# Kernel tuning notes

Measured on AMD Instinct MI355X. Metric: run time of the kernel, lower is better.

The kernel has to match this reference:

```python
import jax, jax.numpy as jnp
from jax import lax
import numpy as np

K = 256   # kernel_size == hidden channels (Haar basis size)
S = 16    # stride
BN_EPS = 1e-5


def _haar_matrix_unnorm(n):
    if n == 2:
        return np.array([[1.0, 1.0], [1.0, -1.0]])
    prev = _haar_matrix_unnorm(n // 2)
    top = np.kron(prev, np.array([1.0, 1.0]))
    bot = np.kron(np.eye(n // 2), np.array([1.0, -1.0]))
    return np.concatenate((top, bot))


def haar_matrix(n):
    h = _haar_matrix_unnorm(n)
    return h / np.linalg.norm(h, axis=1, keepdims=True)


def setup_inputs() -> dict:
    key = jax.random.key(0)
    ks = jax.random.split(key, 8)
    B, T = 64, 32768
    haar = jnp.asarray(haar_matrix(K), dtype=jnp.float32)          # [K, K]
    x = jax.random.normal(ks[0], (B, 1, T), dtype=jnp.float32)
    return {
        "x": x,
        # BitwiseConv1d(1, K, K, stride=S, padding=K)
        "conv_w": haar[:, None, :],                                 # [K, 1, K] (OIH)
        "conv_b": 0.01 * jax.random.normal(ks[1], (K,), dtype=jnp.float32),
        "conv_gate": jax.random.uniform(ks[2], (K, 1, K), dtype=jnp.float32),
        "conv_scale": jnp.ones((K,), dtype=jnp.float32),            # adaptive per-out-channel scale
        # BatchNorm1d(K)
        "bn_gamma": jnp.ones((K,), dtype=jnp.float32),
        "bn_beta": jnp.zeros((K,), dtype=jnp.float32),
        # BitwiseConvTranspose1d(K, 1, K, stride=S)
        "ct_w": haar.T[:, None, :],                                 # [K(in), 1(out), K] (IOH, torch layout)
        "ct_b": 0.01 * jax.random.normal(ks[3], (1,), dtype=jnp.float32),
        "ct_gate": jax.random.uniform(ks[4], (K, 1, K), dtype=jnp.float32),
        "ct_scale": jnp.ones((1,), dtype=jnp.float32),
    }


def _forward(x, conv_w, conv_b, conv_gate, conv_scale, bn_gamma, bn_beta,
             ct_w, ct_b, ct_gate, ct_scale):
    T = x.shape[2]
    # --- BitwiseConv1d: gated weights (in_bin/weight_bin = identity) ---
    # gate binarization maps gate -> (gate + 1) / 2, multiplied into weights
    w = conv_w * (conv_gate + 1.0) * 0.5                            # [K,1,K]
    h = lax.conv_general_dilated(
        x, w, window_strides=(S,), padding=[(K, K)],
        dimension_numbers=("NCH", "OIH", "NCH"))                  # [B,K,L]
    h = conv_scale[None, :, None] * (h + conv_b[None, :, None])    # adaptive scaling
    # --- ReLU then BatchNorm1d (training-mode batch statistics) ---
    h = jax.nn.relu(h)
    mu = jnp.mean(h, axis=(0, 2), keepdims=True)
    var = jnp.mean((h - mu) ** 2, axis=(0, 2), keepdims=True)
    h = (h - mu) * lax.rsqrt(var + BN_EPS)
    h = h * bn_gamma[None, :, None] + bn_beta[None, :, None]
    # --- BitwiseConvTranspose1d: gated weights, expressed as dilated conv ---
    wt = ct_w * (ct_gate + 1.0) * 0.5                               # [K_in, 1, K]
    # torch IOH -> regular-conv OIH with kernel flipped
    wr = jnp.flip(jnp.transpose(wt, (1, 0, 2)), axis=-1)            # [1, K, K]
    y = lax.conv_general_dilated(
        h, wr, window_strides=(1,), padding=[(K - 1, K - 1)],
        lhs_dilation=(S,), dimension_numbers=("NCH", "OIH", "NCH"))
    y = ct_scale[None, :, None] * (y + ct_b[None, :, None])
    # crop: out[:, :, K : T + K]
    return y[:, :, K:T + K]


def reference(x, conv_w, conv_b, conv_gate, conv_scale, bn_gamma, bn_beta,
              ct_w, ct_b, ct_gate, ct_scale):
    return _forward(x, conv_w, conv_b, conv_gate, conv_scale, bn_gamma, bn_beta,
                    ct_w, ct_b, ct_gate, ct_scale)
```

## Files before the change

kernel.cpp:

```cpp
#include <hip/hip_runtime.h>
#include <hip/hip_bf16.h>

#define BB 64
#define TT 32768
#define KK 256
#define LL 2065
#define NLT 9
#define NPART (BB*NLT)
#define NJ 19
#define HBSTR 72
#define NPT3 8

typedef __attribute__((ext_vector_type(8))) short short8;
typedef __attribute__((ext_vector_type(4))) float f32x4;
typedef __attribute__((ext_vector_type(4))) int int4v;
typedef __attribute__((ext_vector_type(2))) unsigned int uint2v;

__device__ __forceinline__ unsigned short f2bf(float f) {
    unsigned u = __builtin_bit_cast(unsigned, f);
    unsigned r = (u + 0x7FFFu + ((u >> 16) & 1u)) >> 16;
    return (unsigned short)r;
}
__device__ __forceinline__ unsigned pkbf(float a, float b) {
    unsigned r;
    asm("v_cvt_pk_bf16_f32 %0, %1, %2" : "=v"(r) : "v"(a), "v"(b));
    return r;
}
__device__ __forceinline__ void gload_lds16(const void* g, void* l) {
    __builtin_amdgcn_global_load_lds(
        (const __attribute__((address_space(1))) unsigned int*)g,
        (__attribute__((address_space(3))) unsigned int*)l, 16, 0, 0);
}

__global__ void k0_w1f(const float* __restrict__ cw, const float* __restrict__ cgt,
                       unsigned short* __restrict__ W1f)
{
    int idx = blockIdx.x*256 + threadIdx.x;
    int lane = idx & 63, ntL = (idx>>6)&7, kk = (idx>>9)&7, half = idx>>12;
    int o = half*128 + ntL*16 + (lane&15);
    int kbase = kk*32 + ((lane>>4)<<3);
    short8 v;
    #pragma unroll
    for (int i = 0; i < 8; ++i) {
        int gi = o*KK + kbase + i;
        v[i] = (short)f2bf(cw[gi]*(cgt[gi]+1.0f)*0.5f);
    }
    *(short8*)(W1f + (size_t)idx*8) = v;
}

__global__ __launch_bounds__(256, 3)
void k1_conv(const float* __restrict__ x, const float* __restrict__ cs,
             const float* __restrict__ cb, const unsigned short* __restrict__ W1f,
             unsigned short* __restrict__ hout,
             float* __restrict__ psum, float* __restrict__ psq)
{
    __shared__ __align__(16) char smem[13056 + 32768];
    char* xwinb = smem;
    char* wbuf  = smem + 13056;
    unsigned short* hb = (unsigned short*)smem;
    float* redS = (float*)(smem + 36864);
    float* redQ = (float*)(smem + 36864 + 1024);

    const int tid   = threadIdx.x;
    const int q     = blockIdx.x & 3;
    const int ltile = blockIdx.x >> 2;
    const int b     = blockIdx.y;
    const int l0    = ltile * 256;
    const long pos0 = (long)l0*16 - 256;
    const int lane  = tid & 63;
    const int w     = tid >> 6;

    {
        #pragma unroll
        for (int it = 0; it < 8; ++it) {
            int ci = w*8 + it;
            int kk = ci >> 2, ntl = ci & 3;
            size_t so = (size_t)((((q>>1)*8 + kk)*8 + (q&1)*4 + ntl))*1024;
            gload_lds16((const char*)W1f + so + lane*16, wbuf + ci*1024);
        }
    }
    {
        const float* xs = x + (size_t)b*TT;
        for (int g = tid; g < 272; g += 256) {
            long base = pos0 + (long)g*16;
            unsigned uu[8];
            if (base >= 0 && base + 16 <= (long)TT) {
                const float4* xv = (const float4*)(xs + base);
                float4 a0 = xv[0], a1 = xv[1], a2 = xv[2], a3 = xv[3];
                uu[0] = pkbf(a0.x, a0.y); uu[1] = pkbf(a0.z, a0.w);
                uu[2] = pkbf(a1.x, a1.y); uu[3] = pkbf(a1.z, a1.w);
                uu[4] = pkbf(a2.x, a2.y); uu[5] = pkbf(a2.z, a2.w);
                uu[6] = pkbf(a3.x, a3.y); uu[7] = pkbf(a3.z, a3.w);
            } else {
                #pragma unroll
                for (int m = 0; m < 16; m += 2) {
                    long p = base + m;
                    float f0 = (p   >= 0 && p   < TT) ? xs[p]   : 0.0f;
                    float f1 = (p+1 >= 0 && p+1 < TT) ? xs[p+1] : 0.0f;
                    uu[m>>1] = pkbf(f0, f1);
                }
            }
            int4v w0 = { (int)uu[0], (int)uu[1], (int)uu[2], (int)uu[3] };
            int4v w1 = { (int)uu[4], (int)uu[5], (int)uu[6], (int)uu[7] };
            *(int4v*)(xwinb + 48*g)      = w0;
            *(int4v*)(xwinb + 48*g + 16) = w1;
        }
    }
    __syncthreads();

    f32x4 acc[4][4];
    #pragma unroll
    for (int mt = 0; mt < 4; ++mt)
        #pragma unroll
        for (int nt = 0; nt < 4; ++nt) acc[mt][nt] = (f32x4){0.f,0.f,0.f,0.f};

    const int gq = lane >> 4;
    const int Gt = 16*gq + 16*(gq>>1);
    const int abase = 48*((w<<6) + (lane & 15)) + Gt;

    #pragma unroll
    for (int kk = 0; kk < 8; ++kk) {
        short8 bfx[4], afw[4];
        #pragma unroll
        for (int nt = 0; nt < 4; ++nt)
            bfx[nt] = *(const short8*)(xwinb + abase + nt*768 + kk*96);
        #pragma unroll
        for (int mt = 0; mt < 4; ++mt)
            afw[mt] = *(const short8*)(wbuf + (kk*4 + mt)*1024 + lane*16);
        __builtin_amdgcn_s_setprio(1);
        #pragma unroll
        for (int mt = 0; mt < 4; ++mt)
            #pragma unroll
            for (int nt = 0; nt < 4; ++nt)
                acc[mt][nt] = __builtin_amdgcn_mfma_f32_16x16x32_bf16(afw[mt], bfx[nt], acc[mt][nt], 0, 0, 0);
        __builtin_amdgcn_s_setprio(0);
    }
    __syncthreads();

    const int c0 = q*64;
    const int g  = lane >> 4;
    const int li = lane & 15;
    #pragma unroll
    for (int mt = 0; mt < 4; ++mt) {
        int cq = c0 + mt*16 + g*4;
        f32x4 cs4 = *(const f32x4*)&cs[cq];
        f32x4 cb4 = *(const f32x4*)&cb[cq];
        f32x4 s4 = (f32x4){0.f,0.f,0.f,0.f};
        f32x4 q4 = (f32x4){0.f,0.f,0.f,0.f};
        #pragma unroll
        for (int nt = 0; nt < 4; ++nt) {
            int lloc = (w<<6) + nt*16 + li;
            f32x4 hv;
            #pragma unroll
            for (int rr = 0; rr < 4; ++rr)
                hv[rr] = fmaxf(cs4[rr]*(acc[mt][nt][rr] + cb4[rr]), 0.0f);
            uint2v pkv = { pkbf(hv[0], hv[1]), pkbf(hv[2], hv[3]) };
            *(uint2v*)(hb + lloc*HBSTR + mt*16 + g*4) = pkv;
            if (l0 + lloc < LL) { s4 += hv; q4 += hv*hv; }
        }
        #pragma unroll
        for (int d = 1; d < 16; d <<= 1) {
            #pragma unroll
            for (int rr = 0; rr < 4; ++rr) {
                s4[rr] += __shfl_xor(s4[rr], d);
                q4[rr] += __shfl_xor(q4[rr], d);
            }
        }
        if (li == 0) {
            *(f32x4*)&redS[((w*4 + mt)*4 + g)*4] = s4;
            *(f32x4*)&redQ[((w*4 + mt)*4 + g)*4] = q4;
        }
    }
    __syncthreads();

    {
        const int rsub = tid >> 3;
        const int cpos = tid & 7;
        #pragma unroll
        for (int it = 0; it < 8; ++it) {
            int row = it*32 + rsub;
            int l = l0 + row;
            if (l < LL) {
                int4v v = *(const int4v*)(hb + row*HBSTR + cpos*8);
                *(int4v*)(hout + (((size_t)(b*LL + l)) << 8) + q*64 + cpos*8) = v;
            }
        }
    }
    if (tid < 64) {
        int mt = tid >> 4, gg = (tid >> 2) & 3, rr = tid & 3;
        float s = 0.f, qq = 0.f;
        #pragma unroll
        for (int wv = 0; wv < 4; ++wv) {
            s  += redS[((wv*4 + mt)*4 + gg)*4 + rr];
            qq += redQ[((wv*4 + mt)*4 + gg)*4 + rr];
        }
        int c = c0 + tid;
        int slot = b*NLT + ltile;
        psum[c*NPART + slot] = s;
        psq [c*NPART + slot] = qq;
    }
}

__global__ __launch_bounds__(256)
void k2_bn(const float* __restrict__ psum, const float* __restrict__ psq,
           const float* __restrict__ bng, const float* __restrict__ bnb,
           const float* __restrict__ ctw, const float* __restrict__ ctg,
           const float* __restrict__ ctscale,
           float* __restrict__ W3s, float* __restrict__ SWS)
{
    __shared__ double rs[4], rq[4];
    __shared__ float s_a, s_bc;
    __shared__ float swl[256];
    const int c = blockIdx.x;
    const int tid = threadIdx.x;
    double s = 0.0, q = 0.0;
    for (int i = tid; i < NPART; i += 256) {
        s += (double)psum[c*NPART + i];
        q += (double)psq [c*NPART + i];
    }
    for (int off = 32; off > 0; off >>= 1) {
        s += __shfl_down(s, off);
        q += __shfl_down(q, off);
    }
    if ((tid & 63) == 0) { rs[tid >> 6] = s; rq[tid >> 6] = q; }
    __syncthreads();
    if (tid == 0) {
        double st = rs[0]+rs[1]+rs[2]+rs[3];
        double qt = rq[0]+rq[1]+rq[2]+rq[3];
        const double cnt = (double)BB * (double)LL;
        double mu = st / cnt;
        double var = qt / cnt - mu*mu;
        float rsig = (float)(1.0 / sqrt(var + 1e-5));
        float a = bng[c] * rsig;
        s_a = a;
        s_bc = bnb[c] - (float)mu * a;
    }
    __syncthreads();
    float a = s_a, bc = s_bc, scl = ctscale[0];
    int gi = c*KK + tid;
    float wt = ctw[gi] * (ctg[gi] + 1.0f) * 0.5f;
    W3s[tid*KK + c] = scl * a * wt;
    swl[tid] = wt * bc;
    __syncthreads();
    if (tid < 16) {
        float acc2 = 0.0f;
        #pragma unroll
        for (int d = 0; d < 16; ++d) acc2 += swl[d*16 + tid];
        SWS[c*16 + tid] = acc2;
    }
}

__global__ void k2b_const(const float* __restrict__ SWS, const float* __restrict__ ctb,
                          const float* __restrict__ ctscale, float* __restrict__ C2)
{
    int r = threadIdx.x;
    if (r < 16) {
        float s = 0.0f;
        for (int c = 0; c < 256; ++c) s += SWS[c*16 + r];
        C2[r] = ctscale[0] * (s + ctb[0]);
    }
}

__global__ void k2c_b2f(const float* __restrict__ W3s, unsigned short* __restrict__ B2f)
{
    int idx = blockIdx.x*256 + threadIdx.x;
    int lane = idx & 63;
    int ntG  = (idx>>6) & 3;
    int kk   = (idx>>8) & 7;
    int j    = idx>>11;
    int c    = kk*32 + ((lane>>4)<<3);
    int r    = lane & 15;
    int d    = ntG + 15 - j;
    short8 v;
    if (d >= 0 && d <= 15) {
        const float* wr = W3s + (size_t)(16*d + r)*KK + c;
        #pragma unroll
        for (int i = 0; i < 8; ++i) v[i] = (short)f2bf(wr[i]);
    } else {
        #pragma unroll
        for (int i = 0; i < 8; ++i) v[i] = 0;
    }
    *(short8*)(B2f + (size_t)idx*8) = v;
}

__global__ __launch_bounds__(512, 1)
void k3_synth(const unsigned short* __restrict__ h, const unsigned short* __restrict__ B2f,
              const float* __restrict__ C2, float* __restrict__ out)
{
    __shared__ __align__(16) char As[272*512];
    const int tid  = threadIdx.x;
    const int lane = tid & 63;
    const int w    = tid >> 6;
    const int b    = blockIdx.y;
    const int P0   = blockIdx.x * 64;

    const char* hbase = (const char*)h + (((size_t)(b*LL) + 4*P0 + 1) << 9);

    {
        const int rl = lane >> 5;
        #pragma unroll
        for (int i = 0; i < 17; ++i) {
            int r0  = w*34 + i*2;
            int row = r0 + rl;
            int chunk = (lane & 31) ^ ((row >> 2) & 7);
            gload_lds16(hbase + (size_t)row*512 + chunk*16, As + r0*512);
        }
    }
    __syncthreads();

    const int ntG = w & 3;
    const int jh  = w >> 2;
    const int li  = lane & 15;
    const int gq  = lane >> 4;

    f32x4 acc[4];
    #pragma unroll
    for (int mt = 0; mt < 4; ++mt) acc[mt] = (f32x4){0.f,0.f,0.f,0.f};

    #pragma unroll 1
    for (int ji = 0; ji < 8; ++ji) {
        const int j = ntG + jh*8 + ji;
        short8 bfr[8];
        #pragma unroll
        for (int kk = 0; kk < 8; ++kk)
            bfr[kk] = *(const short8*)(B2f + (((size_t)(j*8 + kk)*4 + ntG)*64 + lane)*8);
        #pragma unroll
        for (int kk = 0; kk < 8; ++kk) {
            short8 af[4];
            #pragma unroll
            for (int mt = 0; mt < 4; ++mt) {
                int row = 64*mt + 4*li + j;
                int p = (kk*4 + gq) ^ ((row >> 2) & 7);
                af[mt] = *(const short8*)(As + row*512 + p*16);
            }
            __builtin_amdgcn_s_setprio(1);
            #pragma unroll
            for (int mt = 0; mt < 4; ++mt)
                acc[mt] = __builtin_amdgcn_mfma_f32_16x16x32_bf16(af[mt], bfr[kk], acc[mt], 0, 0, 0);
            __builtin_amdgcn_s_setprio(0);
        }
    }
    __syncthreads();

    float* red = (float*)As;
    #pragma unroll
    for (int mt = 0; mt < 4; ++mt) {
        int u = ntG*16 + li;
        #pragma unroll
        for (int rr = 0; rr < 4; ++rr) {
            int Pl = 16*mt + gq*4 + rr;
            red[jh*4352 + Pl*68 + u] = acc[mt][rr];
        }
    }
    __syncthreads();

    {
        const float c2v = C2[tid & 15];
        const int u  = tid & 63;
        const int Pb = tid >> 6;
        float* ob = out + (size_t)b*TT + (size_t)P0*64;
        #pragma unroll
        for (int it = 0; it < 8; ++it) {
            int P = it*8 + Pb;
            ob[P*64 + u] = red[P*68 + u] + red[4352 + P*68 + u] + c2v;
        }
    }
}

extern "C" void kernel_launch(void* const* d_in, const int* in_sizes, int n_in,
                              void* d_out, int out_size, void* d_ws, size_t ws_size,
                              hipStream_t stream)
{
    const float* x       = (const float*)d_in[0];
    const float* cw      = (const float*)d_in[1];
    const float* cb      = (const float*)d_in[2];
    const float* cgt     = (const float*)d_in[3];
    const float* cs      = (const float*)d_in[4];
    const float* bng     = (const float*)d_in[5];
    const float* bnb     = (const float*)d_in[6];
    const float* ctw     = (const float*)d_in[7];
    const float* ctb     = (const float*)d_in[8];
    const float* ctg     = (const float*)d_in[9];
    const float* ctscale = (const float*)d_in[10];
    float* out = (float*)d_out;

    char* ws = (char*)d_ws;
    size_t off = 0;
    unsigned short* h    = (unsigned short*)(ws + off); off += (size_t)BB*LL*KK*2;
    float* psum          = (float*)(ws + off);          off += (size_t)KK*NPART*4;
    float* psq           = (float*)(ws + off);          off += (size_t)KK*NPART*4;
    unsigned short* W1f  = (unsigned short*)(ws + off); off += 65536*2;
    float* W3s           = (float*)(ws + off);          off += (size_t)KK*KK*4;
    float* SWS           = (float*)(ws + off);          off += (size_t)KK*16*4;
    float* C2            = (float*)(ws + off);          off += 64;
    unsigned short* B2f  = (unsigned short*)(ws + off); off += (size_t)NJ*8*4*64*8*2;

    k0_w1f  <<<32, 256, 0, stream>>>(cw, cgt, W1f);
    k1_conv <<<dim3(36, BB), 256, 0, stream>>>(x, cs, cb, W1f, h, psum, psq);
    k2_bn   <<<KK, 256, 0, stream>>>(psum, psq, bng, bnb, ctw, ctg, ctscale, W3s, SWS);
    k2b_const<<<1, 64, 0, stream>>>(SWS, ctb, ctscale, C2);
    k2c_b2f <<<152, 256, 0, stream>>>(W3s, B2f);
    k3_synth<<<dim3(NPT3, BB), 512, 0, stream>>>(h, B2f, C2, out);
}
```

Before: 85.37 us.

## Widen conv tile to 128 channels per block and double-buffer synth weight loads

The first conv kernel now uses 512-thread blocks covering 128 output channels, so each x window is staged and converted once per two channel quarters instead of four. This halves the grid and the redundant x loads, at the cost of more LDS per block and lower occupancy. The synthesis kernel now double-buffers its per-j B fragments in registers, prefetching the next j while computing the current one, which raises register pressure.

After: 93.83 us. 1.1x slower.

```diff
diff --git a/kernel.cpp b/kernel.cpp
--- a/kernel.cpp
+++ b/kernel.cpp
@@ -8,7 +8,7 @@
 #define NLT 9
 #define NPART (BB*NLT)
 #define NJ 19
-#define HBSTR 72
+#define HBSTR 132
 #define NPT3 8
 
 typedef __attribute__((ext_vector_type(8))) short short8;
@@ -48,63 +48,63 @@
     *(short8*)(W1f + (size_t)idx*8) = v;
 }
 
-__global__ __launch_bounds__(256, 3)
+__global__ __launch_bounds__(512, 2)
 void k1_conv(const float* __restrict__ x, const float* __restrict__ cs,
              const float* __restrict__ cb, const unsigned short* __restrict__ W1f,
              unsigned short* __restrict__ hout,
              float* __restrict__ psum, float* __restrict__ psq)
 {
-    __shared__ __align__(16) char smem[13056 + 32768];
+    __shared__ __align__(16) char smem[13056 + 65536];
     char* xwinb = smem;
     char* wbuf  = smem + 13056;
     unsigned short* hb = (unsigned short*)smem;
-    float* redS = (float*)(smem + 36864);
-    float* redQ = (float*)(smem + 36864 + 1024);
+    float* redS = (float*)(smem + 67584);
+    float* redQ = (float*)(smem + 67584 + 2048);
 
     const int tid   = threadIdx.x;
-    const int q     = blockIdx.x & 3;
-    const int ltile = blockIdx.x >> 2;
+    const int half  = blockIdx.x & 1;
+    const int ltile = blockIdx.x >> 1;
     const int b     = blockIdx.y;
     const int l0    = ltile * 256;
     const long pos0 = (long)l0*16 - 256;
     const int lane  = tid & 63;
     const int w     = tid >> 6;
+    const int wq    = w >> 1;
+    const int wc    = w & 1;
 
     {
+        const char* wsrc = (const char*)(W1f + (size_t)half*32768);
         #pragma unroll
         for (int it = 0; it < 8; ++it) {
             int ci = w*8 + it;
-            int kk = ci >> 2, ntl = ci & 3;
-            size_t so = (size_t)((((q>>1)*8 + kk)*8 + (q&1)*4 + ntl))*1024;
-            gload_lds16((const char*)W1f + so + lane*16, wbuf + ci*1024);
-        }
-    }
-    {
+            gload_lds16(wsrc + ci*1024 + lane*16, wbuf + ci*1024);
+        }
+    }
+    if (tid < 272) {
         const float* xs = x + (size_t)b*TT;
-        for (int g = tid; g < 272; g += 256) {
-            long base = pos0 + (long)g*16;
-            unsigned uu[8];
-            if (base >= 0 && base + 16 <= (long)TT) {
-                const float4* xv = (const float4*)(xs + base);
-                float4 a0 = xv[0], a1 = xv[1], a2 = xv[2], a3 = xv[3];
-                uu[0] = pkbf(a0.x, a0.y); uu[1] = pkbf(a0.z, a0.w);
-                uu[2] = pkbf(a1.x, a1.y); uu[3] = pkbf(a1.z, a1.w);
-                uu[4] = pkbf(a2.x, a2.y); uu[5] = pkbf(a2.z, a2.w);
-                uu[6] = pkbf(a3.x, a3.y); uu[7] = pkbf(a3.z, a3.w);
-            } else {
-                #pragma unroll
-                for (int m = 0; m < 16; m += 2) {
-                    long p = base + m;
-                    float f0 = (p   >= 0 && p   < TT) ? xs[p]   : 0.0f;
-                    float f1 = (p+1 >= 0 && p+1 < TT) ? xs[p+1] : 0.0f;
-                    uu[m>>1] = pkbf(f0, f1);
-                }
+        const int g = tid;
+        long base = pos0 + (long)g*16;
+        unsigned uu[8];
+        if (base >= 0 && base + 16 <= (long)TT) {
+            const float4* xv = (const float4*)(xs + base);
+            float4 a0 = xv[0], a1 = xv[1], a2 = xv[2], a3 = xv[3];
+            uu[0] = pkbf(a0.x, a0.y); uu[1] = pkbf(a0.z, a0.w);
+            uu[2] = pkbf(a1.x, a1.y); uu[3] = pkbf(a1.z, a1.w);
+            uu[4] = pkbf(a2.x, a2.y); uu[5] = pkbf(a2.z, a2.w);
+            uu[6] = pkbf(a3.x, a3.y); uu[7] = pkbf(a3.z, a3.w);
+        } else {
+            #pragma unroll
+            for (int m = 0; m < 16; m += 2) {
+                long p = base + m;
+                float f0 = (p   >= 0 && p   < TT) ? xs[p]   : 0.0f;
+                float f1 = (p+1 >= 0 && p+1 < TT) ? xs[p+1] : 0.0f;
+                uu[m>>1] = pkbf(f0, f1);
             }
-            int4v w0 = { (int)uu[0], (int)uu[1], (int)uu[2], (int)uu[3] };
-            int4v w1 = { (int)uu[4], (int)uu[5], (int)uu[6], (int)uu[7] };
-            *(int4v*)(xwinb + 48*g)      = w0;
-            *(int4v*)(xwinb + 48*g + 16) = w1;
-        }
+        }
+        int4v w0 = { (int)uu[0], (int)uu[1], (int)uu[2], (int)uu[3] };
+        int4v w1 = { (int)uu[4], (int)uu[5], (int)uu[6], (int)uu[7] };
+        *(int4v*)(xwinb + 48*g)      = w0;
+        *(int4v*)(xwinb + 48*g + 16) = w1;
     }
     __syncthreads();
 
@@ -116,7 +116,7 @@
 
     const int gq = lane >> 4;
     const int Gt = 16*gq + 16*(gq>>1);
-    const int abase = 48*((w<<6) + (lane & 15)) + Gt;
+    const int abase = 48*((wq<<6) + (lane & 15)) + Gt;
 
     #pragma unroll
     for (int kk = 0; kk < 8; ++kk) {
@@ -126,7 +126,7 @@
             bfx[nt] = *(const short8*)(xwinb + abase + nt*768 + kk*96);
         #pragma unroll
         for (int mt = 0; mt < 4; ++mt)
-            afw[mt] = *(const short8*)(wbuf + (kk*4 + mt)*1024 + lane*16);
+            afw[mt] = *(const short8*)(wbuf + (kk*8 + wc*4 + mt)*1024 + lane*16);
         __builtin_amdgcn_s_setprio(1);
         #pragma unroll
         for (int mt = 0; mt < 4; ++mt)
@@ -137,26 +137,27 @@
     }
     __syncthreads();
 
-    const int c0 = q*64;
     const int g  = lane >> 4;
     const int li = lane & 15;
+    const bool interior = (l0 + 255 < LL);
     #pragma unroll
     for (int mt = 0; mt < 4; ++mt) {
-        int cq = c0 + mt*16 + g*4;
+        int cq = half*128 + wc*64 + mt*16 + g*4;
         f32x4 cs4 = *(const f32x4*)&cs[cq];
         f32x4 cb4 = *(const f32x4*)&cb[cq];
         f32x4 s4 = (f32x4){0.f,0.f,0.f,0.f};
         f32x4 q4 = (f32x4){0.f,0.f,0.f,0.f};
         #pragma unroll
         for (int nt = 0; nt < 4; ++nt) {
-            int lloc = (w<<6) + nt*16 + li;
+            int lloc = (wq<<6) + nt*16 + li;
             f32x4 hv;
             #pragma unroll
             for (int rr = 0; rr < 4; ++rr)
                 hv[rr] = fmaxf(cs4[rr]*(acc[mt][nt][rr] + cb4[rr]), 0.0f);
             uint2v pkv = { pkbf(hv[0], hv[1]), pkbf(hv[2], hv[3]) };
-            *(uint2v*)(hb + lloc*HBSTR + mt*16 + g*4) = pkv;
-            if (l0 + lloc < LL) { s4 += hv; q4 += hv*hv; }
+            *(uint2v*)(hb + lloc*HBSTR + wc*64 + mt*16 + g*4) = pkv;
+            if (interior) { s4 += hv; q4 += hv*hv; }
+            else if (l0 + lloc < LL) { s4 += hv; q4 += hv*hv; }
         }
         #pragma unroll
         for (int d = 1; d < 16; d <<= 1) {
@@ -174,27 +175,28 @@
     __syncthreads();
 
     {
-        const int rsub = tid >> 3;
-        const int cpos = tid & 7;
+        const int rsub = tid >> 4;
+        const int cpos = tid & 15;
         #pragma unroll
         for (int it = 0; it < 8; ++it) {
             int row = it*32 + rsub;
             int l = l0 + row;
             if (l < LL) {
                 int4v v = *(const int4v*)(hb + row*HBSTR + cpos*8);
-                *(int4v*)(hout + (((size_t)(b*LL + l)) << 8) + q*64 + cpos*8) = v;
+                *(int4v*)(hout + (((size_t)(b*LL + l)) << 8) + half*128 + cpos*8) = v;
             }
         }
     }
-    if (tid < 64) {
-        int mt = tid >> 4, gg = (tid >> 2) & 3, rr = tid & 3;
+    if (tid < 128) {
+        int wcc = tid >> 6, mt = (tid >> 4) & 3, gg = (tid >> 2) & 3, rr = tid & 3;
         float s = 0.f, qq = 0.f;
         #pragma unroll
-        for (int wv = 0; wv < 4; ++wv) {
-            s  += redS[((wv*4 + mt)*4 + gg)*4 + rr];
-            qq += redQ[((wv*4 + mt)*4 + gg)*4 + rr];
-        }
-        int c = c0 + tid;
+        for (int wqq = 0; wqq < 4; ++wqq) {
+            int wi = wqq*2 + wcc;
+            s  += redS[((wi*4 + mt)*4 + gg)*4 + rr];
+            qq += redQ[((wi*4 + mt)*4 + gg)*4 + rr];
+        }
+        int c = half*128 + tid;
         int slot = b*NLT + ltile;
         psum[c*NPART + slot] = s;
         psq [c*NPART + slot] = qq;
@@ -312,34 +314,53 @@
     const int jh  = w >> 2;
     const int li  = lane & 15;
     const int gq  = lane >> 4;
+    const int jbase = ntG + jh*8;
 
     f32x4 acc[4];
     #pragma unroll
     for (int mt = 0; mt < 4; ++mt) acc[mt] = (f32x4){0.f,0.f,0.f,0.f};
 
+    short8 bfA[8], bfB[8];
+    #pragma unroll
+    for (int kk = 0; kk < 8; ++kk)
+        bfA[kk] = *(const short8*)(B2f + (((size_t)(jbase*8 + kk)*4 + ntG)*64 + lane)*8);
+
+#define K3_COMPUTE(JV, BF)                                                          \
+    {                                                                               \
+        const int j_ = (JV);                                                        \
+        _Pragma("unroll")                                                           \
+        for (int kk = 0; kk < 8; ++kk) {                                            \
+            short8 af[4];                                                           \
+            _Pragma("unroll")                                                       \
+            for (int mt = 0; mt < 4; ++mt) {                                        \
+                int row = 64*mt + 4*li + j_;                                        \
+                int p = (kk*4 + gq) ^ ((row >> 2) & 7);                             \
+                af[mt] = *(const short8*)(As + row*512 + p*16);                     \
+            }                                                                       \
+            __builtin_amdgcn_s_setprio(1);                                          \
+            _Pragma("unroll")                                                       \
+            for (int mt = 0; mt < 4; ++mt)                                          \
+                acc[mt] = __builtin_amdgcn_mfma_f32_16x16x32_bf16(af[mt], BF[kk],   \
+                                                                  acc[mt], 0, 0, 0);\
+            __builtin_amdgcn_s_setprio(0);                                          \
+        }                                                                           \
+    }
+
     #pragma unroll 1
-    for (int ji = 0; ji < 8; ++ji) {
-        const int j = ntG + jh*8 + ji;
-        short8 bfr[8];
+    for (int jp = 0; jp < 4; ++jp) {
+        const int j0 = jbase + jp*2;
         #pragma unroll
         for (int kk = 0; kk < 8; ++kk)
-            bfr[kk] = *(const short8*)(B2f + (((size_t)(j*8 + kk)*4 + ntG)*64 + lane)*8);
-        #pragma unroll
-        for (int kk = 0; kk < 8; ++kk) {
-            short8 af[4];
+            bfB[kk] = *(const short8*)(B2f + (((size_t)((j0+1)*8 + kk)*4 + ntG)*64 + lane)*8);
+        K3_COMPUTE(j0, bfA);
+        if (jp < 3) {
             #pragma unroll
-            for (int mt = 0; mt < 4; ++mt) {
-                int row = 64*mt + 4*li + j;
-                int p = (kk*4 + gq) ^ ((row >> 2) & 7);
-                af[mt] = *(const short8*)(As + row*512 + p*16);
-            }
-            __builtin_amdgcn_s_setprio(1);
-            #pragma unroll
-            for (int mt = 0; mt < 4; ++mt)
-                acc[mt] = __builtin_amdgcn_mfma_f32_16x16x32_bf16(af[mt], bfr[kk], acc[mt], 0, 0, 0);
-            __builtin_amdgcn_s_setprio(0);
-        }
-    }
+            for (int kk = 0; kk < 8; ++kk)
+                bfA[kk] = *(const short8*)(B2f + (((size_t)((j0+2)*8 + kk)*4 + ntG)*64 + lane)*8);
+        }
+        K3_COMPUTE(j0+1, bfB);
+    }
+#undef K3_COMPUTE
     __syncthreads();
 
     float* red = (float*)As;
@@ -396,7 +417,7 @@
     unsigned short* B2f  = (unsigned short*)(ws + off); off += (size_t)NJ*8*4*64*8*2;
 
     k0_w1f  <<<32, 256, 0, stream>>>(cw, cgt, W1f);
-    k1_conv <<<dim3(36, BB), 256, 0, stream>>>(x, cs, cb, W1f, h, psum, psq);
+    k1_conv <<<dim3(18, BB), 512, 0, stream>>>(x, cs, cb, W1f, h, psum, psq);
     k2_bn   <<<KK, 256, 0, stream>>>(psum, psq, bng, bnb, ctw, ctg, ctscale, W3s, SWS);
     k2b_const<<<1, 64, 0, stream>>>(SWS, ctb, ctscale, C2);
     k2c_b2f <<<152, 256, 0, stream>>>(W3s, B2f);
```

## Split transposed-conv MFMA work by tap per wave with full N tile

Applied to the files above, without the earlier changes.

Each wave now owns a set of taps j and computes all four N tiles, so a single A fragment read from LDS feeds four MFMAs instead of one. B fragments are double-buffered per k-step. The final reduction sums eight per-wave partials with vectorized float4 reads and stores. This cuts LDS A-fragment traffic per MFMA, at the cost of 64 accumulator registers and uneven tap counts across waves (19 taps over 8 waves), plus a larger LDS reduction buffer.

Result: faster. 83.52 us (-2.2%).

```diff
diff --git a/kernel.cpp b/kernel.cpp
--- a/kernel.cpp
+++ b/kernel.cpp
@@ -308,24 +308,30 @@
     }
     __syncthreads();
 
-    const int ntG = w & 3;
-    const int jh  = w >> 2;
-    const int li  = lane & 15;
-    const int gq  = lane >> 4;
-
-    f32x4 acc[4];
-    #pragma unroll
-    for (int mt = 0; mt < 4; ++mt) acc[mt] = (f32x4){0.f,0.f,0.f,0.f};
+    const int li = lane & 15;
+    const int gq = lane >> 4;
+
+    f32x4 acc[4][4];
+    #pragma unroll
+    for (int mt = 0; mt < 4; ++mt)
+        #pragma unroll
+        for (int nt = 0; nt < 4; ++nt) acc[mt][nt] = (f32x4){0.f,0.f,0.f,0.f};
 
     #pragma unroll 1
-    for (int ji = 0; ji < 8; ++ji) {
-        const int j = ntG + jh*8 + ji;
-        short8 bfr[8];
-        #pragma unroll
-        for (int kk = 0; kk < 8; ++kk)
-            bfr[kk] = *(const short8*)(B2f + (((size_t)(j*8 + kk)*4 + ntG)*64 + lane)*8);
+    for (int jj = 0; jj < 3; ++jj) {
+        const int j = w + jj*8;
+        if (j >= NJ) break;
+        short8 bfA[4], bfB[4];
+        #pragma unroll
+        for (int nt = 0; nt < 4; ++nt)
+            bfA[nt] = *(const short8*)(B2f + (((size_t)(j*8 + 0)*4 + nt)*64 + lane)*8);
         #pragma unroll
         for (int kk = 0; kk < 8; ++kk) {
+            if (kk < 7) {
+                #pragma unroll
+                for (int nt = 0; nt < 4; ++nt)
+                    bfB[nt] = *(const short8*)(B2f + (((size_t)(j*8 + kk+1)*4 + nt)*64 + lane)*8);
+            }
             short8 af[4];
             #pragma unroll
             for (int mt = 0; mt < 4; ++mt) {
@@ -336,33 +342,43 @@
             __builtin_amdgcn_s_setprio(1);
             #pragma unroll
             for (int mt = 0; mt < 4; ++mt)
-                acc[mt] = __builtin_amdgcn_mfma_f32_16x16x32_bf16(af[mt], bfr[kk], acc[mt], 0, 0, 0);
+                #pragma unroll
+                for (int nt = 0; nt < 4; ++nt)
+                    acc[mt][nt] = __builtin_amdgcn_mfma_f32_16x16x32_bf16(af[mt], bfA[nt], acc[mt][nt], 0, 0, 0);
             __builtin_amdgcn_s_setprio(0);
+            #pragma unroll
+            for (int nt = 0; nt < 4; ++nt) bfA[nt] = bfB[nt];
         }
     }
     __syncthreads();
 
     float* red = (float*)As;
     #pragma unroll
-    for (int mt = 0; mt < 4; ++mt) {
-        int u = ntG*16 + li;
-        #pragma unroll
-        for (int rr = 0; rr < 4; ++rr) {
-            int Pl = 16*mt + gq*4 + rr;
-            red[jh*4352 + Pl*68 + u] = acc[mt][rr];
-        }
-    }
+    for (int mt = 0; mt < 4; ++mt)
+        #pragma unroll
+        for (int nt = 0; nt < 4; ++nt) {
+            int u = nt*16 + li;
+            #pragma unroll
+            for (int rr = 0; rr < 4; ++rr) {
+                int Pl = 16*mt + gq*4 + rr;
+                red[w*4352 + Pl*68 + u] = acc[mt][nt][rr];
+            }
+        }
     __syncthreads();
 
     {
-        const float c2v = C2[tid & 15];
-        const int u  = tid & 63;
-        const int Pb = tid >> 6;
         float* ob = out + (size_t)b*TT + (size_t)P0*64;
         #pragma unroll
-        for (int it = 0; it < 8; ++it) {
-            int P = it*8 + Pb;
-            ob[P*64 + u] = red[P*68 + u] + red[4352 + P*68 + u] + c2v;
+        for (int it = 0; it < 2; ++it) {
+            int item = it*512 + tid;
+            int P = item >> 4, uq = item & 15;
+            f32x4 s = (f32x4){0.f,0.f,0.f,0.f};
+            #pragma unroll
+            for (int c = 0; c < 8; ++c)
+                s += *(const f32x4*)&red[c*4352 + P*68 + uq*4];
+            int ub = (uq & 3)*4;
+            f32x4 c2v = { C2[ub], C2[ub+1], C2[ub+2], C2[ub+3] };
+            *(f32x4*)&ob[P*64 + uq*4] = s + c2v;
         }
     }
 }
```
